# Performance work log

Measured on AMD Instinct MI355X. Metric: run time of the kernel, lower is better.

The kernel has to match this reference:

```python
import jax, jax.numpy as jnp
import numpy as np

B, C, H, W = 8, 256, 64, 64
NUM_HEADS = 4


def setup_inputs() -> dict:
    key = jax.random.key(0)
    ks = jax.random.split(key, 6)
    s = 0.02  # small init scale for 1x1 conv weights
    return {
        "x": jax.random.normal(ks[0], (B, C, H, W), jnp.float32),
        "cproj": jax.random.normal(ks[1], (B, C, H, W), jnp.float32),
        "wq": jax.random.normal(ks[2], (C, C), jnp.float32) * s,
        "bq": jnp.zeros((C,), jnp.float32),
        "wkv": jax.random.normal(ks[3], (2 * C, C), jnp.float32) * s,
        "bkv": jnp.zeros((2 * C,), jnp.float32),
        "wo": jax.random.normal(ks[4], (C, C), jnp.float32) * s,  # zero_module in torch; random here for a meaningful baseline
        "bo": jnp.zeros((C,), jnp.float32),
    }


def reference(x, cproj, wq, bq, wkv, bkv, wo, bo):
    Bb, Cc, Hh, Ww = x.shape
    N = Hh * Ww
    h = NUM_HEADS
    d = Cc // h
    scale = 1.0 / jnp.sqrt(jnp.sqrt(jnp.asarray(Cc, jnp.float32)))

    xf = x.reshape(Bb, Cc, N)
    cf = cproj.reshape(Bb, Cc, N)

    # 1x1 convs == channel matmuls
    Q = jnp.einsum('oc,bcn->bon', wq, xf) + bq[None, :, None]           # (B,C,N)
    KV = jnp.einsum('oc,bcn->bon', wkv, cf) + bkv[None, :, None]        # (B,2C,N)
    K, V = KV[:, :Cc], KV[:, Cc:]

    # softmax over channel-dim-within-head for q, over spatial N for k
    q = jax.nn.softmax(Q.reshape(Bb, h, d, N) * scale, axis=2).reshape(Bb, Cc, N)
    k = jax.nn.softmax(K.reshape(Bb, h, d, N), axis=3).reshape(Bb, Cc, N)

    # linear-attention: (B,C,C) context, then project back to N — note heads are mixed, per original bmm
    context = jnp.einsum('bcn,bdn->bcd', k, V)
    out = jnp.einsum('bcd,bdn->bcn', context, q)

    out = jnp.einsum('oc,bcn->bon', wo, out) + bo[None, :, None]
    return out.reshape(Bb, Cc, Hh, Ww)
```

## Files before the change

kernel.cpp:

```cpp
#include <hip/hip_runtime.h>

#define B_ 8
#define C_ 256
#define N_ 4096
#define NSPLIT 16

typedef float f32x4 __attribute__((ext_vector_type(4)));
typedef __bf16 bf16x8 __attribute__((ext_vector_type(8)));
typedef __bf16 bf16x4 __attribute__((ext_vector_type(4)));
typedef unsigned short u16x8 __attribute__((ext_vector_type(8)));
typedef unsigned short u16x4 __attribute__((ext_vector_type(4)));

__device__ __forceinline__ unsigned short f2bf(float f) {
  return __builtin_bit_cast(unsigned short, (__bf16)f);
}
__device__ __forceinline__ float bf2f(unsigned short u) {
  return __uint_as_float((unsigned)u << 16);
}

__device__ __forceinline__ f32x4 mfma16(bf16x8 a, bf16x8 b, f32x4 c) {
  return __builtin_amdgcn_mfma_f32_16x16x32_bf16(a, b, c, 0, 0, 0);
}

typedef __attribute__((address_space(1))) const void* gvp;
typedef __attribute__((address_space(3))) void* lvp;
__device__ __forceinline__ void gld16(const void* g, void* l) {
  __builtin_amdgcn_global_load_lds((gvp)g, (lvp)l, 16, 0, 0);
}

template <int ROWS>
__device__ __forceinline__ void stage(unsigned short* lds, const unsigned short* g,
                                      int ld, int w, int lane) {
  const int r8 = lane >> 3;
  const int ce = ((lane & 7) ^ r8) << 3;
  const unsigned short* gp = g + (size_t)(w * (ROWS / 4) + r8) * ld + ce;
  unsigned short* lp = lds + w * (ROWS / 4) * 64;
#pragma unroll
  for (int i = 0; i < ROWS / 32; i++)
    gld16(gp + (size_t)(i * 8) * ld, lp + i * 512);
}

__device__ __forceinline__ bf16x8 frag(const unsigned short* lds, int row, int kc) {
  return *(const bf16x8*)(lds + row * 64 + ((kc ^ (row & 7)) << 3));
}

__device__ __forceinline__ void loadB(float4* pbv, const float* src, int ld,
                                      int n0, int kt, int w, int lane) {
  const int nf = lane & 15, kg = lane >> 4;
  const float* sp = src + (size_t)(kt * 64 + w * 16 + kg * 4) * ld + n0 + 4 * nf;
#pragma unroll
  for (int h = 0; h < 2; h++)
#pragma unroll
    for (int i = 0; i < 4; i++)
      pbv[h * 4 + i] = *(const float4*)(sp + h * 64 + (size_t)i * ld);
}
__device__ __forceinline__ void writeB(unsigned short* Bs, const float4* pbv,
                                       int w, int lane) {
  const int nf = lane & 15, kg = lane >> 4;
  const int k0 = w * 16 + kg * 4;
#pragma unroll
  for (int h = 0; h < 2; h++)
#pragma unroll
    for (int j = 0; j < 4; j++) {
      bf16x4 o = (bf16x4){(__bf16)((const float*)&pbv[h * 4 + 0])[j],
                          (__bf16)((const float*)&pbv[h * 4 + 1])[j],
                          (__bf16)((const float*)&pbv[h * 4 + 2])[j],
                          (__bf16)((const float*)&pbv[h * 4 + 3])[j]};
      *(bf16x4*)&Bs[(h * 64 + 4 * nf + j) * 68 + k0] = o;
    }
}
__device__ __forceinline__ bf16x8 fragB(const unsigned short* Bs, int n, int k8) {
  union { u16x4 q[2]; bf16x8 b; } u;
  const unsigned short* p = Bs + n * 68 + k8 * 8;
  u.q[0] = *(const u16x4*)p;
  u.q[1] = *(const u16x4*)(p + 4);
  return u.b;
}

__device__ __forceinline__ bf16x8 fragC(const unsigned short* Ct, int n, int k8) {
  union { u16x4 q[2]; bf16x8 b; } u;
  const unsigned short* p = Ct + n * 268 + k8 * 8;
  u.q[0] = *(const u16x4*)p;
  u.q[1] = *(const u16x4*)(p + 4);
  return u.b;
}

__global__ __launch_bounds__(256) void castw(
    const float* __restrict__ wq, const float* __restrict__ wkv,
    const float* __restrict__ wo, unsigned short* __restrict__ wqb,
    unsigned short* __restrict__ wkvb, unsigned short* __restrict__ wob,
    float* __restrict__ Z) {
  int t = blockIdx.x * 256 + threadIdx.x;
  if (t < B_ * C_) Z[t] = 0.f;
  int i = t * 4;
  const float* src;
  unsigned short* dst;
  int off;
  if (i < 65536) { src = wq; dst = wqb; off = i; }
  else if (i < 196608) { src = wkv; dst = wkvb; off = i - 65536; }
  else { src = wo; dst = wob; off = i - 196608; }
  float4 v = *(const float4*)(src + off);
  *(u16x4*)(dst + off) = (u16x4){f2bf(v.x), f2bf(v.y), f2bf(v.z), f2bf(v.w)};
}

__device__ __forceinline__ void qproj_body(
    unsigned short* As, unsigned short* Bs, const unsigned short* __restrict__ wqb,
    const float* __restrict__ x, const float* __restrict__ bq,
    unsigned short* __restrict__ qT, int b, int n0, int m0b) {
  const int tid = threadIdx.x, lane = tid & 63, w = tid >> 6;
  const int m0w = (w >> 1) * 64;
  const int n0w = (w & 1) * 64;
  const int colL = lane & 15, kq = lane >> 4, quad = lane >> 4;
  const float* xb = x + (size_t)b * C_ * N_;

  f32x4 acc[4][4];
#pragma unroll
  for (int i = 0; i < 4; i++)
#pragma unroll
    for (int j = 0; j < 4; j++) acc[i][j] = (f32x4){0.f, 0.f, 0.f, 0.f};

  float4 pbv[8];
  loadB(pbv, xb, N_, n0, 0, w, lane);

  for (int kt = 0; kt < 4; kt++) {
    writeB(Bs, pbv, w, lane);
    stage<128>(As, wqb + (size_t)m0b * C_ + kt * 64, C_, w, lane);
    __syncthreads();
    if (kt < 3) loadB(pbv, xb, N_, n0, kt + 1, w, lane);
#pragma unroll
    for (int ks = 0; ks < 2; ks++) {
      bf16x8 af[4], bf[4];
#pragma unroll
      for (int mt = 0; mt < 4; mt++) af[mt] = frag(As, m0w + mt * 16 + colL, ks * 4 + kq);
#pragma unroll
      for (int nt = 0; nt < 4; nt++) bf[nt] = fragB(Bs, n0w + nt * 16 + colL, ks * 4 + kq);
#pragma unroll
      for (int mt = 0; mt < 4; mt++)
#pragma unroll
        for (int nt = 0; nt < 4; nt++) acc[mt][nt] = mfma16(af[mt], bf[nt], acc[mt][nt]);
    }
    __syncthreads();
  }

#pragma unroll
  for (int nt = 0; nt < 4; nt++) {
    float v[16];
    float mx = -1e30f;
#pragma unroll
    for (int mt = 0; mt < 4; mt++)
#pragma unroll
      for (int r = 0; r < 4; r++) {
        int m = m0b + m0w + mt * 16 + quad * 4 + r;
        float val = (acc[mt][nt][r] + bq[m]) * 0.25f;
        v[mt * 4 + r] = val;
        mx = fmaxf(mx, val);
      }
    mx = fmaxf(mx, __shfl_xor(mx, 16));
    mx = fmaxf(mx, __shfl_xor(mx, 32));
    float s = 0.f;
#pragma unroll
    for (int j = 0; j < 16; j++) { v[j] = __expf(v[j] - mx); s += v[j]; }
    s += __shfl_xor(s, 16);
    s += __shfl_xor(s, 32);
    float inv = 1.0f / s;
    const int n = n0 + n0w + nt * 16 + colL;
    unsigned short* qb = qT + ((size_t)b * N_ + n) * C_ + m0b + m0w;
#pragma unroll
    for (int mt = 0; mt < 4; mt++) {
      u16x4 o = (u16x4){f2bf(v[mt * 4 + 0] * inv), f2bf(v[mt * 4 + 1] * inv),
                        f2bf(v[mt * 4 + 2] * inv), f2bf(v[mt * 4 + 3] * inv)};
      *(u16x4*)(qb + mt * 16 + quad * 4) = o;
    }
  }
}

__device__ __forceinline__ void kvproj_body(
    unsigned short* As, unsigned short* Bs, const unsigned short* __restrict__ wkvb,
    const float* __restrict__ cp, const float* __restrict__ bkv,
    unsigned short* __restrict__ Eb, unsigned short* __restrict__ Vb,
    float* __restrict__ Z, int b, int n0, int m0b) {
  const int tid = threadIdx.x, lane = tid & 63, w = tid >> 6;
  const int m0w = w * 32;
  const int colL = lane & 15, kq = lane >> 4, quad = lane >> 4;
  const float* cpb = cp + (size_t)b * C_ * N_;

  f32x4 acc[2][8];
#pragma unroll
  for (int i = 0; i < 2; i++)
#pragma unroll
    for (int j = 0; j < 8; j++) acc[i][j] = (f32x4){0.f, 0.f, 0.f, 0.f};

  float4 pbv[8];
  loadB(pbv, cpb, N_, n0, 0, w, lane);

  for (int kt = 0; kt < 4; kt++) {
    writeB(Bs, pbv, w, lane);
    stage<128>(As, wkvb + (size_t)m0b * C_ + kt * 64, C_, w, lane);
    __syncthreads();
    if (kt < 3) loadB(pbv, cpb, N_, n0, kt + 1, w, lane);
#pragma unroll
    for (int ks = 0; ks < 2; ks++) {
      bf16x8 bf[8];
#pragma unroll
      for (int nt = 0; nt < 8; nt++) bf[nt] = fragB(Bs, nt * 16 + colL, ks * 4 + kq);
#pragma unroll
      for (int mt = 0; mt < 2; mt++) {
        bf16x8 af = frag(As, m0w + mt * 16 + colL, ks * 4 + kq);
#pragma unroll
        for (int nt = 0; nt < 8; nt++) acc[mt][nt] = mfma16(af, bf[nt], acc[mt][nt]);
      }
    }
    __syncthreads();
  }

#pragma unroll
  for (int mt = 0; mt < 2; mt++)
#pragma unroll
    for (int r = 0; r < 4; r++) {
      int m = m0b + m0w + mt * 16 + quad * 4 + r;
      float bias = bkv[m];
      if (m < C_) {
        unsigned short* er = Eb + ((size_t)b * C_ + m) * N_ + n0;
        float es = 0.f;
#pragma unroll
        for (int nt = 0; nt < 8; nt++) {
          float e = __expf(acc[mt][nt][r] + bias);
          er[nt * 16 + colL] = f2bf(e);
          es += e;
        }
        es += __shfl_xor(es, 1);
        es += __shfl_xor(es, 2);
        es += __shfl_xor(es, 4);
        es += __shfl_xor(es, 8);
        if ((lane & 15) == 0) atomicAdd(&Z[b * C_ + m], es);
      } else {
        unsigned short* vr = Vb + ((size_t)b * C_ + m - C_) * N_ + n0;
#pragma unroll
        for (int nt = 0; nt < 8; nt++) vr[nt * 16 + colL] = f2bf(acc[mt][nt][r] + bias);
      }
    }
}

__global__ __launch_bounds__(256) void qkvproj(
    const unsigned short* __restrict__ wqb, const unsigned short* __restrict__ wkvb,
    const float* __restrict__ x, const float* __restrict__ cp,
    const float* __restrict__ bq, const float* __restrict__ bkv,
    unsigned short* __restrict__ qT, unsigned short* __restrict__ Eb,
    unsigned short* __restrict__ Vb, float* __restrict__ Z) {
  __shared__ __align__(16) unsigned short As[128 * 64];
  __shared__ __align__(16) unsigned short Bs[128 * 68];
  const int b = blockIdx.z, n0 = blockIdx.x * 128;
  if (blockIdx.y < 2)
    qproj_body(As, Bs, wqb, x, bq, qT, b, n0, blockIdx.y * 128);
  else
    kvproj_body(As, Bs, wkvb, cp, bkv, Eb, Vb, Z, b, n0, (blockIdx.y - 2) * 128);
}

__global__ __launch_bounds__(256) void ctx_part(
    const unsigned short* __restrict__ Eb, const float* __restrict__ Z,
    const unsigned short* __restrict__ Vb, unsigned short* __restrict__ ctxp) {
  __shared__ __align__(16) unsigned short As[128 * 64];
  __shared__ __align__(16) unsigned short Bs[128 * 64];
  const int bid = blockIdx.x;
  const int swz = (bid & 7) * 64 + (bid >> 3);
  const int b = swz >> 6, r = swz & 63;
  const int s = r >> 2;
  const int m0 = ((r >> 1) & 1) * 128, n0 = (r & 1) * 128;
  const int tid = threadIdx.x, lane = tid & 63, w = tid >> 6;
  const int m0w = (w & 1) * 64, n0w = (w >> 1) * 64;
  const int colL = lane & 15, kq = lane >> 4, quad = lane >> 4;
  const unsigned short* Ag = Eb + ((size_t)b * C_ + m0) * N_;
  const unsigned short* Bg = Vb + ((size_t)b * C_ + n0) * N_;
  const int kbeg = s * (N_ / NSPLIT);

  f32x4 acc[4][4];
#pragma unroll
  for (int i = 0; i < 4; i++)
#pragma unroll
    for (int j = 0; j < 4; j++) acc[i][j] = (f32x4){0.f, 0.f, 0.f, 0.f};

  for (int kt = 0; kt < (N_ / NSPLIT) / 64; kt++) {
    stage<128>(As, Ag + kbeg + kt * 64, N_, w, lane);
    stage<128>(Bs, Bg + kbeg + kt * 64, N_, w, lane);
    __syncthreads();
#pragma unroll
    for (int ks = 0; ks < 2; ks++) {
      bf16x8 af[4], bf[4];
#pragma unroll
      for (int mt = 0; mt < 4; mt++) af[mt] = frag(As, m0w + mt * 16 + colL, ks * 4 + kq);
#pragma unroll
      for (int nt = 0; nt < 4; nt++) bf[nt] = frag(Bs, n0w + nt * 16 + colL, ks * 4 + kq);
#pragma unroll
      for (int mt = 0; mt < 4; mt++)
#pragma unroll
        for (int nt = 0; nt < 4; nt++) acc[mt][nt] = mfma16(af[mt], bf[nt], acc[mt][nt]);
    }
    __syncthreads();
  }

  unsigned short* outp = ctxp + ((size_t)s * B_ + b) * C_ * C_;
  const float* Zb = Z + b * C_;
#pragma unroll
  for (int mt = 0; mt < 4; mt++)
#pragma unroll
    for (int r2 = 0; r2 < 4; r2++) {
      int m = m0 + m0w + mt * 16 + quad * 4 + r2;
      float iz = 1.0f / Zb[m];
#pragma unroll
      for (int nt = 0; nt < 4; nt++) {
        int n = n0 + n0w + nt * 16 + colL;
        outp[(size_t)m * C_ + n] = f2bf(acc[mt][nt][r2] * iz);
      }
    }
}

__global__ __launch_bounds__(256) void ctxoproj(
    const unsigned short* __restrict__ ctxp, const unsigned short* __restrict__ wob,
    unsigned short* __restrict__ ctx2) {
  __shared__ __align__(16) unsigned short AsW[4 * 64 * 64];
  __shared__ __align__(16) unsigned short Ct[32 * 268];
  const int bid = blockIdx.x;
  const int swz = (bid & 7) * 32 + (bid >> 3);
  const int b = swz >> 5, r = swz & 31;
  const int o0 = (r >> 3) * 64, d0 = (r & 7) * 32;
  const int tid = threadIdx.x, lane = tid & 63, w = tid >> 6;
  const int colL = lane & 15, kq = lane >> 4, quad = lane >> 4;

#pragma unroll
  for (int ck = 0; ck < 4; ck++)
    stage<64>(AsW + ck * 4096, wob + (size_t)o0 * C_ + ck * 64, C_, w, lane);

  const int q = tid & 7, cl = tid >> 3;
  const unsigned short* pb = ctxp + ((size_t)b * C_ + cl) * C_ + d0 + q * 4;
#pragma unroll 2
  for (int p = 0; p < 8; p++) {
    f32x4 s4 = (f32x4){0.f, 0.f, 0.f, 0.f};
    const unsigned short* pp = pb + (size_t)p * 32 * C_;
#pragma unroll
    for (int s = 0; s < NSPLIT; s++) {
      u16x4 v = *(const u16x4*)(pp + (size_t)s * B_ * C_ * C_);
      s4[0] += bf2f(v[0]); s4[1] += bf2f(v[1]);
      s4[2] += bf2f(v[2]); s4[3] += bf2f(v[3]);
    }
    const int c = p * 32 + cl;
#pragma unroll
    for (int j = 0; j < 4; j++) Ct[(q * 4 + j) * 268 + c] = f2bf(s4[j]);
  }
  __syncthreads();

  f32x4 acc2[2];
  acc2[0] = (f32x4){0.f, 0.f, 0.f, 0.f};
  acc2[1] = (f32x4){0.f, 0.f, 0.f, 0.f};
#pragma unroll
  for (int kt = 0; kt < 4; kt++)
#pragma unroll
    for (int ks = 0; ks < 2; ks++) {
      bf16x8 af = frag(AsW + kt * 4096, w * 16 + colL, ks * 4 + kq);
#pragma unroll
      for (int nt = 0; nt < 2; nt++) {
        bf16x8 bf = fragC(Ct, nt * 16 + colL, kt * 8 + ks * 4 + kq);
        acc2[nt] = mfma16(af, bf, acc2[nt]);
      }
    }
  unsigned short* ob = ctx2 + (size_t)b * C_ * C_;
#pragma unroll
  for (int nt = 0; nt < 2; nt++)
#pragma unroll
    for (int r2 = 0; r2 < 4; r2++)
      ob[(size_t)(o0 + w * 16 + quad * 4 + r2) * C_ + d0 + nt * 16 + colL] =
          f2bf(acc2[nt][r2]);
}

__global__ __launch_bounds__(256) void outgemm(
    const unsigned short* __restrict__ ctx2, const unsigned short* __restrict__ qT,
    const float* __restrict__ bo, float* __restrict__ out) {
  __shared__ __align__(16) unsigned short As[128 * 64];
  __shared__ __align__(16) unsigned short Bs[64 * 64];
  const int bid = blockIdx.x;
  const int swz = (bid & 7) * 128 + (bid >> 3);
  const int b = swz >> 7, r = swz & 127;
  const int m0b = (r >> 6) * 128, n0 = (r & 63) * 64;
  const int tid = threadIdx.x, lane = tid & 63, w = tid >> 6;
  const int m0w = w * 32;
  const int colL = lane & 15, kq = lane >> 4, quad = lane >> 4;
  const unsigned short* Ag = ctx2 + (size_t)b * C_ * C_ + (size_t)m0b * C_;
  const unsigned short* Bg = qT + ((size_t)b * N_ + n0) * C_;

  f32x4 acc[2][4];
#pragma unroll
  for (int i = 0; i < 2; i++)
#pragma unroll
    for (int j = 0; j < 4; j++) acc[i][j] = (f32x4){0.f, 0.f, 0.f, 0.f};

  for (int kt = 0; kt < 4; kt++) {
    stage<128>(As, Ag + kt * 64, C_, w, lane);
    stage<64>(Bs, Bg + kt * 64, C_, w, lane);
    __syncthreads();
#pragma unroll
    for (int ks = 0; ks < 2; ks++) {
      bf16x8 af[2], bf[4];
#pragma unroll
      for (int mt = 0; mt < 2; mt++) af[mt] = frag(As, m0w + mt * 16 + colL, ks * 4 + kq);
#pragma unroll
      for (int nt = 0; nt < 4; nt++) bf[nt] = frag(Bs, nt * 16 + colL, ks * 4 + kq);
#pragma unroll
      for (int mt = 0; mt < 2; mt++)
#pragma unroll
        for (int nt = 0; nt < 4; nt++) acc[mt][nt] = mfma16(af[mt], bf[nt], acc[mt][nt]);
    }
    __syncthreads();
  }

  float* ob = out + (size_t)b * C_ * N_;
#pragma unroll
  for (int mt = 0; mt < 2; mt++)
#pragma unroll
    for (int r2 = 0; r2 < 4; r2++) {
      int m = m0b + m0w + mt * 16 + quad * 4 + r2;
      float bias = bo[m];
#pragma unroll
      for (int nt = 0; nt < 4; nt++) {
        int n = n0 + nt * 16 + colL;
        ob[(size_t)m * N_ + n] = acc[mt][nt][r2] + bias;
      }
    }
}

extern "C" void kernel_launch(void* const* d_in, const int* in_sizes, int n_in,
                              void* d_out, int out_size, void* d_ws, size_t ws_size,
                              hipStream_t stream) {
  const float* x     = (const float*)d_in[0];
  const float* cproj = (const float*)d_in[1];
  const float* wq    = (const float*)d_in[2];
  const float* bq    = (const float*)d_in[3];
  const float* wkv   = (const float*)d_in[4];
  const float* bkv   = (const float*)d_in[5];
  const float* wo    = (const float*)d_in[6];
  const float* bo    = (const float*)d_in[7];
  float* out = (float*)d_out;

  unsigned short* qT    = (unsigned short*)d_ws;
  unsigned short* Eb    = qT + 8388608;
  unsigned short* Vb    = Eb + 8388608;
  unsigned short* ctxp  = Vb + 8388608;
  unsigned short* wqb   = ctxp + 8388608;
  unsigned short* wkvb  = wqb + 65536;
  unsigned short* wob   = wkvb + 131072;
  unsigned short* ctx2  = wob + 65536;
  float*          Zbuf  = (float*)(ctx2 + 524288);

  castw<<<256, 256, 0, stream>>>(wq, wkv, wo, wqb, wkvb, wob, Zbuf);
  qkvproj<<<dim3(32, 6, 8), 256, 0, stream>>>(wqb, wkvb, x, cproj, bq, bkv,
                                              qT, Eb, Vb, Zbuf);
  ctx_part<<<512, 256, 0, stream>>>(Eb, Zbuf, Vb, ctxp);
  ctxoproj<<<256, 256, 0, stream>>>(ctxp, wob, ctx2);
  outgemm<<<1024, 256, 0, stream>>>(ctx2, qT, bo, out);
}
```

Baseline: 181.1 us.

## Double-buffer LDS staging in ctx_part and outgemm with explicit vmcnt waits

Converts the K-loop in the context-partial and output GEMM kernels to a two-stage LDS double buffer. The next tile is prefetched with global_load_lds while the current one is consumed, using explicit s_waitcnt vmcnt counts and raw barriers in place of __syncthreads. This overlaps global-to-LDS latency with MFMA work in these short 4-iteration loops. The cost is twice the LDS per block, which may lower occupancy, and the hand-set vmcnt values must match the number of loads each stage issues.

```diff
diff --git a/kernel.cpp b/kernel.cpp
--- a/kernel.cpp
+++ b/kernel.cpp
@@ -27,6 +27,10 @@
 __device__ __forceinline__ void gld16(const void* g, void* l) {
   __builtin_amdgcn_global_load_lds((gvp)g, (lvp)l, 16, 0, 0);
 }
+
+#define VMWAIT(N) do { asm volatile("s_waitcnt vmcnt(" #N ")" ::: "memory"); \
+                       __builtin_amdgcn_sched_barrier(0); } while (0)
+#define BAR() __builtin_amdgcn_s_barrier()
 
 template <int ROWS>
 __device__ __forceinline__ void stage(unsigned short* lds, const unsigned short* g,
@@ -259,8 +263,8 @@
 __global__ __launch_bounds__(256) void ctx_part(
     const unsigned short* __restrict__ Eb, const float* __restrict__ Z,
     const unsigned short* __restrict__ Vb, unsigned short* __restrict__ ctxp) {
-  __shared__ __align__(16) unsigned short As[128 * 64];
-  __shared__ __align__(16) unsigned short Bs[128 * 64];
+  __shared__ __align__(16) unsigned short As[2][128 * 64];
+  __shared__ __align__(16) unsigned short Bs[2][128 * 64];
   const int bid = blockIdx.x;
   const int swz = (bid & 7) * 64 + (bid >> 3);
   const int b = swz >> 6, r = swz & 63;
@@ -269,9 +273,8 @@
   const int tid = threadIdx.x, lane = tid & 63, w = tid >> 6;
   const int m0w = (w & 1) * 64, n0w = (w >> 1) * 64;
   const int colL = lane & 15, kq = lane >> 4, quad = lane >> 4;
-  const unsigned short* Ag = Eb + ((size_t)b * C_ + m0) * N_;
-  const unsigned short* Bg = Vb + ((size_t)b * C_ + n0) * N_;
-  const int kbeg = s * (N_ / NSPLIT);
+  const unsigned short* Ag = Eb + ((size_t)b * C_ + m0) * N_ + s * (N_ / NSPLIT);
+  const unsigned short* Bg = Vb + ((size_t)b * C_ + n0) * N_ + s * (N_ / NSPLIT);
 
   f32x4 acc[4][4];
 #pragma unroll
@@ -279,23 +282,38 @@
 #pragma unroll
     for (int j = 0; j < 4; j++) acc[i][j] = (f32x4){0.f, 0.f, 0.f, 0.f};
 
-  for (int kt = 0; kt < (N_ / NSPLIT) / 64; kt++) {
-    stage<128>(As, Ag + kbeg + kt * 64, N_, w, lane);
-    stage<128>(Bs, Bg + kbeg + kt * 64, N_, w, lane);
-    __syncthreads();
+  stage<128>(As[0], Ag + 0 * 64, N_, w, lane);
+  stage<128>(Bs[0], Bg + 0 * 64, N_, w, lane);
+  stage<128>(As[1], Ag + 1 * 64, N_, w, lane);
+  stage<128>(Bs[1], Bg + 1 * 64, N_, w, lane);
+  VMWAIT(8);
+  BAR();
+
+  for (int kt = 0; kt < 4; kt++) {
+    const unsigned short* Asc = As[kt & 1];
+    const unsigned short* Bsc = Bs[kt & 1];
 #pragma unroll
     for (int ks = 0; ks < 2; ks++) {
       bf16x8 af[4], bf[4];
 #pragma unroll
-      for (int mt = 0; mt < 4; mt++) af[mt] = frag(As, m0w + mt * 16 + colL, ks * 4 + kq);
-#pragma unroll
-      for (int nt = 0; nt < 4; nt++) bf[nt] = frag(Bs, n0w + nt * 16 + colL, ks * 4 + kq);
+      for (int mt = 0; mt < 4; mt++) af[mt] = frag(Asc, m0w + mt * 16 + colL, ks * 4 + kq);
+#pragma unroll
+      for (int nt = 0; nt < 4; nt++) bf[nt] = frag(Bsc, n0w + nt * 16 + colL, ks * 4 + kq);
 #pragma unroll
       for (int mt = 0; mt < 4; mt++)
 #pragma unroll
         for (int nt = 0; nt < 4; nt++) acc[mt][nt] = mfma16(af[mt], bf[nt], acc[mt][nt]);
     }
-    __syncthreads();
+    if (kt == 3) break;
+    BAR();
+    if (kt + 2 < 4) {
+      stage<128>(As[kt & 1], Ag + (kt + 2) * 64, N_, w, lane);
+      stage<128>(Bs[kt & 1], Bg + (kt + 2) * 64, N_, w, lane);
+      VMWAIT(8);
+    } else {
+      VMWAIT(0);
+    }
+    BAR();
   }
 
   unsigned short* outp = ctxp + ((size_t)s * B_ + b) * C_ * C_;
@@ -374,8 +392,8 @@
 __global__ __launch_bounds__(256) void outgemm(
     const unsigned short* __restrict__ ctx2, const unsigned short* __restrict__ qT,
     const float* __restrict__ bo, float* __restrict__ out) {
-  __shared__ __align__(16) unsigned short As[128 * 64];
-  __shared__ __align__(16) unsigned short Bs[64 * 64];
+  __shared__ __align__(16) unsigned short As[2][128 * 64];
+  __shared__ __align__(16) unsigned short Bs[2][64 * 64];
   const int bid = blockIdx.x;
   const int swz = (bid & 7) * 128 + (bid >> 3);
   const int b = swz >> 7, r = swz & 127;
@@ -392,23 +410,38 @@
 #pragma unroll
     for (int j = 0; j < 4; j++) acc[i][j] = (f32x4){0.f, 0.f, 0.f, 0.f};
 
+  stage<128>(As[0], Ag + 0 * 64, C_, w, lane);
+  stage<64>(Bs[0], Bg + 0 * 64, C_, w, lane);
+  stage<128>(As[1], Ag + 1 * 64, C_, w, lane);
+  stage<64>(Bs[1], Bg + 1 * 64, C_, w, lane);
+  VMWAIT(6);
+  BAR();
+
   for (int kt = 0; kt < 4; kt++) {
-    stage<128>(As, Ag + kt * 64, C_, w, lane);
-    stage<64>(Bs, Bg + kt * 64, C_, w, lane);
-    __syncthreads();
+    const unsigned short* Asc = As[kt & 1];
+    const unsigned short* Bsc = Bs[kt & 1];
 #pragma unroll
     for (int ks = 0; ks < 2; ks++) {
       bf16x8 af[2], bf[4];
 #pragma unroll
-      for (int mt = 0; mt < 2; mt++) af[mt] = frag(As, m0w + mt * 16 + colL, ks * 4 + kq);
-#pragma unroll
-      for (int nt = 0; nt < 4; nt++) bf[nt] = frag(Bs, nt * 16 + colL, ks * 4 + kq);
+      for (int mt = 0; mt < 2; mt++) af[mt] = frag(Asc, m0w + mt * 16 + colL, ks * 4 + kq);
+#pragma unroll
+      for (int nt = 0; nt < 4; nt++) bf[nt] = frag(Bsc, nt * 16 + colL, ks * 4 + kq);
 #pragma unroll
       for (int mt = 0; mt < 2; mt++)
 #pragma unroll
         for (int nt = 0; nt < 4; nt++) acc[mt][nt] = mfma16(af[mt], bf[nt], acc[mt][nt]);
     }
-    __syncthreads();
+    if (kt == 3) break;
+    BAR();
+    if (kt + 2 < 4) {
+      stage<128>(As[kt & 1], Ag + (kt + 2) * 64, C_, w, lane);
+      stage<64>(Bs[kt & 1], Bg + (kt + 2) * 64, C_, w, lane);
+      VMWAIT(6);
+    } else {
+      VMWAIT(0);
+    }
+    BAR();
   }
 
   float* ob = out + (size_t)b * C_ * N_;
```

Measured after the change: 181.4 us, median of 2. Within noise of the previous version (+0.1%).
